# Kernel optimization log

Hardware: AMD Instinct MI355X
Metric: run time of the kernel (lower is better)

The kernel has to match this reference:

```python
import jax, jax.numpy as jnp
import numpy as np
from jax import lax

K = 16        # patch_size / kernel_size
S = 16        # stride
EMB = 768     # embed_dim
CIN = 3


def setup_inputs() -> dict:
    key = jax.random.key(0)
    k1, k2, k3, k4, k5 = jax.random.split(key, 5)
    B, H, W = 64, 384, 384
    pixel_values = jax.random.normal(k1, (B, CIN, H, W), jnp.float32)
    # offset conv: Conv2d(3, 2*K*K, kernel=K, stride=K); small init so offsets stay moderate
    offset_w = jax.random.normal(k2, (2 * K * K, CIN, K, K), jnp.float32) * 0.01
    offset_b = jax.random.normal(k3, (2 * K * K,), jnp.float32) * 0.01
    # deformable projection: DeformConv2d(3, 768, kernel=K, stride=K)
    proj_w = jax.random.normal(k4, (EMB, CIN, K, K), jnp.float32) * 0.02
    proj_b = jax.random.normal(k5, (EMB,), jnp.float32) * 0.02
    return {"pixel_values": pixel_values, "offset_w": offset_w, "offset_b": offset_b,
            "proj_w": proj_w, "proj_b": proj_b}


def _bilinear_gather(img, py, px):
    """img: [B,C,H,W]; py,px: [B,K,K,HO,WO] float sample coords.
    Returns [B,C,K,K,HO,WO] with zero padding outside the image (torchvision semantics)."""
    B, C, H, W = img.shape
    shp = py.shape
    y0 = jnp.floor(py); x0 = jnp.floor(px)
    wy1 = py - y0; wy0 = 1.0 - wy1
    wx1 = px - x0; wx0 = 1.0 - wx1
    imgf = img.reshape(B, C, H * W)

    def corner(yy, xx, w):
        valid = (yy >= 0) & (yy < H) & (xx >= 0) & (xx < W)
        yi = jnp.clip(yy, 0, H - 1).astype(jnp.int32)
        xi = jnp.clip(xx, 0, W - 1).astype(jnp.int32)
        idx = (yi * W + xi).reshape(B, -1)                       # [B, N]
        v = jnp.take_along_axis(imgf, idx[:, None, :], axis=2)   # [B, C, N]
        return v * (jnp.where(valid, w, 0.0)).reshape(B, 1, -1)

    val = (corner(y0, x0, wy0 * wx0) + corner(y0, x0 + 1, wy0 * wx1)
           + corner(y0 + 1, x0, wy1 * wx0) + corner(y0 + 1, x0 + 1, wy1 * wx1))
    return val.reshape((B, C) + shp[1:])


def reference(pixel_values, offset_w, offset_b, proj_w, proj_b):
    B, C, H, W = pixel_values.shape
    HO, WO = H // S, W // S
    # offset conv (dense, stride=patch, VALID padding)
    offset = lax.conv_general_dilated(pixel_values, offset_w, (S, S), 'VALID',
                                      dimension_numbers=('NCHW', 'OIHW', 'NCHW'))
    offset = offset + offset_b[None, :, None, None]              # [B, 2*K*K, HO, WO]
    off = offset.reshape(B, K * K, 2, HO, WO)
    dy = off[:, :, 0].reshape(B, K, K, HO, WO)
    dx = off[:, :, 1].reshape(B, K, K, HO, WO)
    # base sampling grid: p = (ho*S + i + dy, wo*S + j + dx)
    base_y = (jnp.arange(HO, dtype=jnp.float32) * S)[None, None, None, :, None] \
             + jnp.arange(K, dtype=jnp.float32)[None, :, None, None, None]
    base_x = (jnp.arange(WO, dtype=jnp.float32) * S)[None, None, None, None, :] \
             + jnp.arange(K, dtype=jnp.float32)[None, None, :, None, None]
    py = base_y + dy
    px = base_x + dx
    sampled = _bilinear_gather(pixel_values, py, px)             # [B, C, K, K, HO, WO]
    out = jnp.einsum('bcijhw,ocij->bohw', sampled, proj_w) + proj_b[None, :, None, None]
    # flatten(2).transpose(1,2) -> [B, HO*WO, EMB]
    return out.reshape(B, EMB, HO * WO).transpose(0, 2, 1)
```

## Files before the change

### kernel.cpp

```cpp
#include <hip/hip_runtime.h>
#include <stdint.h>

typedef __bf16 bf16x8 __attribute__((ext_vector_type(8)));
typedef float  f32x4  __attribute__((ext_vector_type(4)));

#define HH 384
#define WW 384
#define NPIX (HH*WW)
#define NC 3
#define NPATCH 576
#define EMB 768
#define PLEN 768
#define KSTEPS 24
#define NLOC (64*576)
#define W1_UNITS (32*KSTEPS*64)
#define W2_UNITS (48*KSTEPS*64)
#define W2_OFF   (W1_UNITS*8)
#define AP_OFF   ((W1_UNITS+W2_UNITS)*8)
#define SA_OFF   (AP_OFF + NLOC*PLEN)
#define P0_WBLKS ((W1_UNITS+W2_UNITS)/256)
#define P0_BANDS (64*24)

__device__ __forceinline__ uint16_t f2bf(float f) {
    uint32_t u = __builtin_bit_cast(uint32_t, f);
    u += 0x7FFFu + ((u >> 16) & 1u);
    return (uint16_t)(u >> 16);
}
__device__ __forceinline__ uint32_t pk2(float a, float b) {
    return (uint32_t)f2bf(a) | ((uint32_t)f2bf(b) << 16);
}
__device__ __forceinline__ float bf2f(uint16_t u) {
    return __builtin_bit_cast(float, (uint32_t)u << 16);
}

__global__ __launch_bounds__(256)
void p0_prepass(const float* __restrict__ offw, const float* __restrict__ projw,
                const float* __restrict__ pix, uint16_t* __restrict__ wz) {
    __shared__ uint16_t L[3 * 16 * 384];
    int b = blockIdx.x;
    if (b < P0_WBLKS) {
        int u = b * 256 + threadIdx.x;
        const float* src;
        int uu;
        if (u < W1_UNITS) { src = offw; uu = u; }
        else              { src = projw; uu = u - W1_UNITS; }
        int lane = uu & 63;
        int t    = uu >> 6;
        int ks   = t % KSTEPS;
        int nt   = t / KSTEPS;
        int n    = nt * 16 + (lane & 15);
        int k0   = ks * 32 + (lane >> 4) * 8;
        const float4* s4 = (const float4*)(src + (size_t)n * PLEN + k0);
        float4 v0 = s4[0], v1 = s4[1];
        uint4 w;
        w.x = pk2(v0.x, v0.y); w.y = pk2(v0.z, v0.w);
        w.z = pk2(v1.x, v1.y); w.w = pk2(v1.z, v1.w);
        *(uint4*)(wz + (size_t)u * 8) = w;
        return;
    }
    int band = b - P0_WBLKS;
    int img  = band / 24;
    int yb   = band - img * 24;
    const float* src = pix + (size_t)img * NC * NPIX + (size_t)yb * 16 * WW;
    #pragma unroll
    for (int i = 0; i < 18; ++i) {
        int u = threadIdx.x + i * 256;
        int c = u / 1536;
        int r = u - c * 1536;
        float4 v = *(const float4*)(src + (size_t)c * NPIX + (size_t)r * 4);
        uint2 o;
        o.x = pk2(v.x, v.y);
        o.y = pk2(v.z, v.w);
        *(uint2*)&L[c * 6144 + r * 4] = o;
    }
    __syncthreads();
    uint16_t* ap = wz + AP_OFF + (size_t)(img * NPATCH + yb * 24) * PLEN;
    #pragma unroll
    for (int i = 0; i < 9; ++i) {
        int u  = threadIdx.x + i * 256;
        int p  = u / 96;
        int k8 = (u - p * 96) * 8;
        int c  = k8 >> 8;
        int ii = (k8 >> 4) & 15;
        int j  = k8 & 15;
        uint4 d = *(const uint4*)&L[(c * 16 + ii) * 384 + p * 16 + j];
        *(uint4*)(ap + (size_t)p * PLEN + k8) = d;
    }
}

__global__ __launch_bounds__(256, 3)
void k1_offgemm(const uint16_t* __restrict__ wz, const float* __restrict__ offb,
                uint16_t* __restrict__ sa) {
    __shared__ __align__(16) uint16_t Asb[2][128][64];
    const int tid = threadIdx.x, wv = tid >> 6, lane = tid & 63;
    const int lr = lane & 15, lg = lane >> 4;
    const int wm = wv >> 1, wn = wv & 1;
    int bid = (int)blockIdx.x;
    const int fin   = (bid & 7) * 144 + (bid >> 3);
    const int mtile = fin >> 2;
    const int nc    = fin & 3;
    const int loc0  = mtile * 128;
    const int n0    = nc * 128;
    const uint16_t* __restrict__ Ap = wz + AP_OFF;

    const uint16_t* gs[4];
    #pragma unroll
    for (int l = 0; l < 4; ++l) {
        int u = l * 256 + tid;
        int row = u >> 3, ch = u & 7;
        gs[l] = Ap + (size_t)(loc0 + row) * PLEN + (ch ^ (row & 7)) * 8;
    }
    auto stage = [&](int t, int buf) {
        #pragma unroll
        for (int l = 0; l < 4; ++l)
            __builtin_amdgcn_global_load_lds(
                (const uint32_t*)(gs[l] + t * 64),
                (uint32_t*)((uint16_t*)&Asb[buf][0][0] + (size_t)(l * 256 + wv * 64) * 8),
                16, 0, 0);
    };
    auto ldb = [&](int nt, int ks) -> bf16x8 {
        int ntg = nc * 8 + wn * 4 + nt;
        return *(const bf16x8*)(wz + ((size_t)((ntg * KSTEPS + ks) * 64 + lane)) * 8);
    };

    f32x4 acc[4][4];
    #pragma unroll
    for (int nt = 0; nt < 4; ++nt) {
        float bz = offb[n0 + wn * 64 + nt * 16 + lr];
        f32x4 z = {bz, bz, bz, bz};
        #pragma unroll
        for (int mi = 0; mi < 4; ++mi) acc[mi][nt] = z;
    }

    bf16x8 ba[4], bb[4];
    stage(0, 0);
    #pragma unroll
    for (int nt = 0; nt < 4; ++nt) ba[nt] = ldb(nt, 0);
    __syncthreads();

    #pragma unroll 1
    for (int t = 0; t < 12; ++t) {
        const int cur = t & 1;
        if (t < 11) stage(t + 1, cur ^ 1);
        {
            #pragma unroll
            for (int nt = 0; nt < 4; ++nt) bb[nt] = ldb(nt, 2 * t + 1);
            const int u0 = (lg ^ (lr & 7)) * 8;
            bf16x8 a0 = *(const bf16x8*)&Asb[cur][wm * 64 +  0 + lr][u0];
            bf16x8 a1 = *(const bf16x8*)&Asb[cur][wm * 64 + 16 + lr][u0];
            bf16x8 a2 = *(const bf16x8*)&Asb[cur][wm * 64 + 32 + lr][u0];
            bf16x8 a3 = *(const bf16x8*)&Asb[cur][wm * 64 + 48 + lr][u0];
            #pragma unroll
            for (int nt = 0; nt < 4; ++nt) {
                acc[0][nt] = __builtin_amdgcn_mfma_f32_16x16x32_bf16(a0, ba[nt], acc[0][nt], 0, 0, 0);
                acc[1][nt] = __builtin_amdgcn_mfma_f32_16x16x32_bf16(a1, ba[nt], acc[1][nt], 0, 0, 0);
                acc[2][nt] = __builtin_amdgcn_mfma_f32_16x16x32_bf16(a2, ba[nt], acc[2][nt], 0, 0, 0);
                acc[3][nt] = __builtin_amdgcn_mfma_f32_16x16x32_bf16(a3, ba[nt], acc[3][nt], 0, 0, 0);
            }
        }
        {
            if (t < 11) {
                #pragma unroll
                for (int nt = 0; nt < 4; ++nt) ba[nt] = ldb(nt, 2 * t + 2);
            }
            const int u1 = ((4 + lg) ^ (lr & 7)) * 8;
            bf16x8 a0 = *(const bf16x8*)&Asb[cur][wm * 64 +  0 + lr][u1];
            bf16x8 a1 = *(const bf16x8*)&Asb[cur][wm * 64 + 16 + lr][u1];
            bf16x8 a2 = *(const bf16x8*)&Asb[cur][wm * 64 + 32 + lr][u1];
            bf16x8 a3 = *(const bf16x8*)&Asb[cur][wm * 64 + 48 + lr][u1];
            #pragma unroll
            for (int nt = 0; nt < 4; ++nt) {
                acc[0][nt] = __builtin_amdgcn_mfma_f32_16x16x32_bf16(a0, bb[nt], acc[0][nt], 0, 0, 0);
                acc[1][nt] = __builtin_amdgcn_mfma_f32_16x16x32_bf16(a1, bb[nt], acc[1][nt], 0, 0, 0);
                acc[2][nt] = __builtin_amdgcn_mfma_f32_16x16x32_bf16(a2, bb[nt], acc[2][nt], 0, 0, 0);
                acc[3][nt] = __builtin_amdgcn_mfma_f32_16x16x32_bf16(a3, bb[nt], acc[3][nt], 0, 0, 0);
            }
        }
        __syncthreads();
    }

    #pragma unroll
    for (int nt = 0; nt < 4; ++nt)
      #pragma unroll
      for (int mi = 0; mi < 4; ++mi)
        #pragma unroll
        for (int r = 0; r < 4; ++r) {
            float v  = acc[mi][nt][r];
            float pv = __shfl_xor(v, 1);
            if ((lane & 1) == 0) {
                int row = loc0 + wm * 64 + mi * 16 + lg * 4 + r;
                int q   = (n0 >> 1) + wn * 32 + nt * 8 + (lr >> 1);
                ((uint32_t*)(sa + (size_t)row * PLEN))[q] = pk2(v, pv);
            }
        }
}

__global__ __launch_bounds__(512)
void k2_gather(const uint16_t* __restrict__ wz, uint16_t* __restrict__ sa) {
    const int tid  = threadIdx.x;
    const int wv   = tid >> 6;
    const int lane = tid & 63;
    int bid = (int)blockIdx.x;
    const int tile = (bid & 7) * 144 + (bid >> 3);
    const int loc0 = tile * 32;
    const int bimg = loc0 / NPATCH;
    const int p0   = loc0 - bimg * NPATCH;
    const uint16_t* __restrict__ apim = wz + AP_OFF + (size_t)bimg * NPATCH * PLEN;

    #pragma unroll
    for (int li = 0; li < 4; ++li) {
        const int L   = wv * 4 + li;
        const int p   = p0 + L;
        const int ho  = p / 24;
        const int wo  = p - ho * 24;
        const int by  = ho * 16;
        const int bx  = wo * 16;
        uint16_t* row = sa + (size_t)(loc0 + L) * PLEN;
        const uint32_t* rowu = (const uint32_t*)row;
        uint32_t od0 = rowu[       lane];
        uint32_t od1 = rowu[ 64 +  lane];
        uint32_t od2 = rowu[128 +  lane];
        uint32_t od3 = rowu[192 +  lane];
        asm volatile("s_waitcnt vmcnt(0)" ::: "memory");
        #pragma unroll
        for (int s4 = 0; s4 < 4; ++s4) {
            const int q  = s4 * 64 + lane;
            const int qi = q >> 4;
            const int qj = q & 15;
            uint32_t od = (s4 == 0) ? od0 : (s4 == 1) ? od1 : (s4 == 2) ? od2 : od3;
            float dy = bf2f((uint16_t)od);
            float dx = bf2f((uint16_t)(od >> 16));
            float py = (float)(by + qi) + dy;
            float px = (float)(bx + qj) + dx;
            float y0f = floorf(py), x0f = floorf(px);
            float wy1 = py - y0f, wy0 = 1.f - wy1;
            float wx1 = px - x0f, wx0 = 1.f - wx1;
            int y0 = (int)y0f, x0 = (int)x0f;
            float s0 = 0.f, s1 = 0.f, s2 = 0.f;
            #pragma unroll
            for (int cy = 0; cy < 2; ++cy) {
                int yy = y0 + cy;
                if ((unsigned)yy < (unsigned)HH) {
                    float wy = cy ? wy1 : wy0;
                    #pragma unroll
                    for (int cx = 0; cx < 2; ++cx) {
                        int xx = x0 + cx;
                        if ((unsigned)xx < (unsigned)WW) {
                            float w = wy * (cx ? wx1 : wx0);
                            int pp = (yy >> 4) * 24 + (xx >> 4);
                            const uint16_t* cp = apim + (size_t)pp * PLEN
                                               + (((yy & 15) << 4) | (xx & 15));
                            s0 += w * bf2f(cp[0]);
                            s1 += w * bf2f(cp[256]);
                            s2 += w * bf2f(cp[512]);
                        }
                    }
                }
            }
            row[      q] = f2bf(s0);
            row[256 + q] = f2bf(s1);
            row[512 + q] = f2bf(s2);
        }
    }
}

__global__ __launch_bounds__(256, 3)
void k3_proj(const uint16_t* __restrict__ wz, const float* __restrict__ projb,
             float* __restrict__ out) {
    __shared__ __align__(16) uint16_t Asb[2][128][64];
    const int tid = threadIdx.x, wv = tid >> 6, lane = tid & 63;
    const int lr = lane & 15, lg = lane >> 4;
    const int wm = wv >> 1, wn = wv & 1;
    int bid = (int)blockIdx.x;
    const int fin   = (bid & 7) * 216 + (bid >> 3);
    const int mtile = fin / 6;
    const int ncol  = fin - mtile * 6;
    const int loc0  = mtile * 128;
    const int n0    = ncol * 128;
    const uint16_t* __restrict__ sa = wz + SA_OFF;

    const uint16_t* gs[4];
    #pragma unroll
    for (int l = 0; l < 4; ++l) {
        int u = l * 256 + tid;
        int row = u >> 3, ch = u & 7;
        gs[l] = sa + (size_t)(loc0 + row) * PLEN + (ch ^ (row & 7)) * 8;
    }
    auto stage = [&](int t, int buf) {
        #pragma unroll
        for (int l = 0; l < 4; ++l)
            __builtin_amdgcn_global_load_lds(
                (const uint32_t*)(gs[l] + t * 64),
                (uint32_t*)((uint16_t*)&Asb[buf][0][0] + (size_t)(l * 256 + wv * 64) * 8),
                16, 0, 0);
    };
    auto ldb = [&](int nt, int ks) -> bf16x8 {
        int ntg = ncol * 8 + wn * 4 + nt;
        return *(const bf16x8*)(wz + W2_OFF + ((size_t)((ntg * KSTEPS + ks) * 64 + lane)) * 8);
    };

    f32x4 acc[4][4];
    #pragma unroll
    for (int nt = 0; nt < 4; ++nt) {
        float bz = projb[n0 + wn * 64 + nt * 16 + lr];
        f32x4 z = {bz, bz, bz, bz};
        #pragma unroll
        for (int mi = 0; mi < 4; ++mi) acc[mi][nt] = z;
    }

    bf16x8 ba[4], bb[4];
    stage(0, 0);
    #pragma unroll
    for (int nt = 0; nt < 4; ++nt) ba[nt] = ldb(nt, 0);
    __syncthreads();

    #pragma unroll 1
    for (int t = 0; t < 12; ++t) {
        const int cur = t & 1;
        if (t < 11) stage(t + 1, cur ^ 1);
        {
            #pragma unroll
            for (int nt = 0; nt < 4; ++nt) bb[nt] = ldb(nt, 2 * t + 1);
            const int u0 = (lg ^ (lr & 7)) * 8;
            bf16x8 a0 = *(const bf16x8*)&Asb[cur][wm * 64 +  0 + lr][u0];
            bf16x8 a1 = *(const bf16x8*)&Asb[cur][wm * 64 + 16 + lr][u0];
            bf16x8 a2 = *(const bf16x8*)&Asb[cur][wm * 64 + 32 + lr][u0];
            bf16x8 a3 = *(const bf16x8*)&Asb[cur][wm * 64 + 48 + lr][u0];
            #pragma unroll
            for (int nt = 0; nt < 4; ++nt) {
                acc[0][nt] = __builtin_amdgcn_mfma_f32_16x16x32_bf16(a0, ba[nt], acc[0][nt], 0, 0, 0);
                acc[1][nt] = __builtin_amdgcn_mfma_f32_16x16x32_bf16(a1, ba[nt], acc[1][nt], 0, 0, 0);
                acc[2][nt] = __builtin_amdgcn_mfma_f32_16x16x32_bf16(a2, ba[nt], acc[2][nt], 0, 0, 0);
                acc[3][nt] = __builtin_amdgcn_mfma_f32_16x16x32_bf16(a3, ba[nt], acc[3][nt], 0, 0, 0);
            }
        }
        {
            if (t < 11) {
                #pragma unroll
                for (int nt = 0; nt < 4; ++nt) ba[nt] = ldb(nt, 2 * t + 2);
            }
            const int u1 = ((4 + lg) ^ (lr & 7)) * 8;
            bf16x8 a0 = *(const bf16x8*)&Asb[cur][wm * 64 +  0 + lr][u1];
            bf16x8 a1 = *(const bf16x8*)&Asb[cur][wm * 64 + 16 + lr][u1];
            bf16x8 a2 = *(const bf16x8*)&Asb[cur][wm * 64 + 32 + lr][u1];
            bf16x8 a3 = *(const bf16x8*)&Asb[cur][wm * 64 + 48 + lr][u1];
            #pragma unroll
            for (int nt = 0; nt < 4; ++nt) {
                acc[0][nt] = __builtin_amdgcn_mfma_f32_16x16x32_bf16(a0, bb[nt], acc[0][nt], 0, 0, 0);
                acc[1][nt] = __builtin_amdgcn_mfma_f32_16x16x32_bf16(a1, bb[nt], acc[1][nt], 0, 0, 0);
                acc[2][nt] = __builtin_amdgcn_mfma_f32_16x16x32_bf16(a2, bb[nt], acc[2][nt], 0, 0, 0);
                acc[3][nt] = __builtin_amdgcn_mfma_f32_16x16x32_bf16(a3, bb[nt], acc[3][nt], 0, 0, 0);
            }
        }
        __syncthreads();
    }

    #pragma unroll
    for (int mi = 0; mi < 4; ++mi)
      #pragma unroll
      for (int r = 0; r < 4; ++r) {
        int rowg = loc0 + wm * 64 + mi * 16 + lg * 4 + r;
        float* op = out + (size_t)rowg * EMB + n0 + wn * 64;
        #pragma unroll
        for (int nt = 0; nt < 4; ++nt)
            op[nt * 16 + lr] = acc[mi][nt][r];
      }
}

__global__ __launch_bounds__(256)
void fallback_kernel(const float* __restrict__ pix, const float* __restrict__ offw,
                     const float* __restrict__ offb, const float* __restrict__ projw,
                     const float* __restrict__ projb, float* __restrict__ out) {
    __shared__ float buf[8][PLEN];
    const int tid = threadIdx.x;
    const int loc0 = blockIdx.x * 8;
    #pragma unroll
    for (int r = 0; r < 6; ++r) {
        int item = tid + r * 256;
        int l = item / 192, k = (item - l * 192) * 4;
        int c = k >> 8, i = (k >> 4) & 15, j = k & 15;
        int flat = loc0 + l, b = flat / NPATCH, p = flat - b * NPATCH;
        int ho = p / 24, wo = p - ho * 24;
        *(float4*)(&buf[l][k]) = *(const float4*)(pix +
            (((size_t)b * NC + c) * HH + (size_t)ho * 16 + i) * WW + wo * 16 + j);
    }
    __syncthreads();
    float dy[8], dx[8];
    {
        float a0[8], a1[8];
        float b0 = offb[2 * tid], b1 = offb[2 * tid + 1];
        #pragma unroll
        for (int l = 0; l < 8; ++l) { a0[l] = b0; a1[l] = b1; }
        const float4* w0 = (const float4*)(offw + (size_t)(2 * tid) * PLEN);
        const float4* w1 = w0 + PLEN / 4;
        for (int k4 = 0; k4 < PLEN / 4; ++k4) {
            float4 wa = w0[k4], wb = w1[k4];
            #pragma unroll
            for (int l = 0; l < 8; ++l) {
                float4 pv = *(const float4*)(&buf[l][k4 * 4]);
                a0[l] += wa.x*pv.x + wa.y*pv.y + wa.z*pv.z + wa.w*pv.w;
                a1[l] += wb.x*pv.x + wb.y*pv.y + wb.z*pv.z + wb.w*pv.w;
            }
        }
        #pragma unroll
        for (int l = 0; l < 8; ++l) { dy[l] = a0[l]; dx[l] = a1[l]; }
    }
    __syncthreads();
    {
        const int i = tid >> 4, j = tid & 15;
        #pragma unroll
        for (int l = 0; l < 8; ++l) {
            int flat = loc0 + l, b = flat / NPATCH, p = flat - b * NPATCH;
            int ho = p / 24, wo = p - ho * 24;
            float py = (float)(ho * 16 + i) + dy[l];
            float px = (float)(wo * 16 + j) + dx[l];
            float y0 = floorf(py), x0 = floorf(px);
            float wy1 = py - y0, wy0 = 1.f - wy1, wx1 = px - x0, wx0 = 1.f - wx1;
            const float* pb = pix + (size_t)b * NC * NPIX;
            float s0 = 0, s1 = 0, s2 = 0;
            #pragma unroll
            for (int cy = 0; cy < 2; ++cy)
              #pragma unroll
              for (int cx = 0; cx < 2; ++cx) {
                int yy = (int)y0 + cy, xx = (int)x0 + cx;
                float w = (cy ? wy1 : wy0) * (cx ? wx1 : wx0);
                if ((unsigned)yy < (unsigned)HH && (unsigned)xx < (unsigned)WW) {
                    int idx = yy * WW + xx;
                    s0 += w * pb[idx]; s1 += w * pb[NPIX + idx]; s2 += w * pb[2*NPIX + idx];
                }
              }
            buf[l][tid] = s0; buf[l][256 + tid] = s1; buf[l][512 + tid] = s2;
        }
    }
    __syncthreads();
    {
        float aA[8], aB[8], aC[8];
        float bA = projb[tid], bB = projb[tid + 256], bC = projb[tid + 512];
        #pragma unroll
        for (int l = 0; l < 8; ++l) { aA[l] = bA; aB[l] = bB; aC[l] = bC; }
        const float4* wA = (const float4*)(projw + (size_t)tid * PLEN);
        const float4* wB = (const float4*)(projw + (size_t)(tid + 256) * PLEN);
        const float4* wC = (const float4*)(projw + (size_t)(tid + 512) * PLEN);
        for (int k4 = 0; k4 < PLEN / 4; ++k4) {
            float4 a = wA[k4], bq = wB[k4], cq = wC[k4];
            #pragma unroll
            for (int l = 0; l < 8; ++l) {
                float4 pv = *(const float4*)(&buf[l][k4 * 4]);
                aA[l] += a.x*pv.x + a.y*pv.y + a.z*pv.z + a.w*pv.w;
                aB[l] += bq.x*pv.x + bq.y*pv.y + bq.z*pv.z + bq.w*pv.w;
                aC[l] += cq.x*pv.x + cq.y*pv.y + cq.z*pv.z + cq.w*pv.w;
            }
        }
        #pragma unroll
        for (int l = 0; l < 8; ++l) {
            float* op = out + (size_t)(loc0 + l) * EMB;
            op[tid] = aA[l]; op[tid + 256] = aB[l]; op[tid + 512] = aC[l];
        }
    }
}

extern "C" void kernel_launch(void* const* d_in, const int* in_sizes, int n_in,
                              void* d_out, int out_size, void* d_ws, size_t ws_size,
                              hipStream_t stream) {
    const float* pix   = (const float*)d_in[0];
    const float* offw  = (const float*)d_in[1];
    const float* offb  = (const float*)d_in[2];
    const float* projw = (const float*)d_in[3];
    const float* projb = (const float*)d_in[4];
    float* out = (float*)d_out;
    uint16_t* wz = (uint16_t*)d_ws;

    const size_t ws_needed = ((size_t)SA_OFF + (size_t)NLOC * PLEN) * 2;

    if (ws_size >= ws_needed) {
        uint16_t* sa = wz + SA_OFF;
        p0_prepass<<<P0_WBLKS + P0_BANDS, 256, 0, stream>>>(offw, projw, pix, wz);
        k1_offgemm<<<1152, 256, 0, stream>>>(wz, offb, sa);
        k2_gather<<<1152, 512, 0, stream>>>(wz, sa);
        k3_proj<<<1728, 256, 0, stream>>>(wz, projb, out);
    } else {
        fallback_kernel<<<NLOC / 8, 256, 0, stream>>>(pix, offw, offb, projw, projb, out);
    }
}
```

Baseline: 205.2 us.

## Interleave channels in patch layout so bilinear gather loads all three in two words

Changes the K dimension ordering of the patch matrix and offset weights from channel-major (c*256+q) to channel-interleaved (q*3+c), applied consistently in the prepass for both the offset weights and the pixel patches. The bilinear sampler can then fetch all three channels of a corner with two adjacent 32-bit loads instead of three loads spaced 512 bytes apart. In exchange the prepass does scalar strided LDS reads and scalar global loads for the offset weights rather than vector loads, and the sampler adds shift and select logic for odd alignment.

```diff
diff --git a/kernel.cpp b/kernel.cpp
--- a/kernel.cpp
+++ b/kernel.cpp
@@ -40,22 +40,41 @@
     int b = blockIdx.x;
     if (b < P0_WBLKS) {
         int u = b * 256 + threadIdx.x;
-        const float* src;
-        int uu;
-        if (u < W1_UNITS) { src = offw; uu = u; }
-        else              { src = projw; uu = u - W1_UNITS; }
-        int lane = uu & 63;
-        int t    = uu >> 6;
-        int ks   = t % KSTEPS;
-        int nt   = t / KSTEPS;
-        int n    = nt * 16 + (lane & 15);
-        int k0   = ks * 32 + (lane >> 4) * 8;
-        const float4* s4 = (const float4*)(src + (size_t)n * PLEN + k0);
-        float4 v0 = s4[0], v1 = s4[1];
-        uint4 w;
-        w.x = pk2(v0.x, v0.y); w.y = pk2(v0.z, v0.w);
-        w.z = pk2(v1.x, v1.y); w.w = pk2(v1.z, v1.w);
-        *(uint4*)(wz + (size_t)u * 8) = w;
+        int lane = u & 63;
+        if (u < W1_UNITS) {
+            int t  = u >> 6;
+            int ks = t % KSTEPS;
+            int nt = t / KSTEPS;
+            int n  = nt * 16 + (lane & 15);
+            int k0 = ks * 32 + (lane >> 4) * 8;
+            const float* src = offw + (size_t)n * PLEN;
+            uint16_t tmp[8];
+            #pragma unroll
+            for (int e = 0; e < 8; ++e) {
+                int k = k0 + e;
+                int q = k / 3, c = k - q * 3;
+                tmp[e] = f2bf(src[c * 256 + q]);
+            }
+            uint4 w;
+            w.x = tmp[0] | ((uint32_t)tmp[1] << 16);
+            w.y = tmp[2] | ((uint32_t)tmp[3] << 16);
+            w.z = tmp[4] | ((uint32_t)tmp[5] << 16);
+            w.w = tmp[6] | ((uint32_t)tmp[7] << 16);
+            *(uint4*)(wz + (size_t)u * 8) = w;
+        } else {
+            int uu = u - W1_UNITS;
+            int t2 = uu >> 6;
+            int ks = t2 % KSTEPS;
+            int nt = t2 / KSTEPS;
+            int n  = nt * 16 + (lane & 15);
+            int k0 = ks * 32 + (lane >> 4) * 8;
+            const float4* s4 = (const float4*)(projw + (size_t)n * PLEN + k0);
+            float4 v0 = s4[0], v1 = s4[1];
+            uint4 w;
+            w.x = pk2(v0.x, v0.y); w.y = pk2(v0.z, v0.w);
+            w.z = pk2(v1.x, v1.y); w.w = pk2(v1.z, v1.w);
+            *(uint4*)(wz + (size_t)u * 8) = w;
+        }
         return;
     }
     int band = b - P0_WBLKS;
@@ -80,10 +99,19 @@
         int u  = threadIdx.x + i * 256;
         int p  = u / 96;
         int k8 = (u - p * 96) * 8;
-        int c  = k8 >> 8;
-        int ii = (k8 >> 4) & 15;
-        int j  = k8 & 15;
-        uint4 d = *(const uint4*)&L[(c * 16 + ii) * 384 + p * 16 + j];
+        uint16_t tmp[8];
+        #pragma unroll
+        for (int e = 0; e < 8; ++e) {
+            int k = k8 + e;
+            int q = k / 3, c = k - q * 3;
+            int ii = q >> 4, j = q & 15;
+            tmp[e] = L[(c * 16 + ii) * 384 + p * 16 + j];
+        }
+        uint4 d;
+        d.x = tmp[0] | ((uint32_t)tmp[1] << 16);
+        d.y = tmp[2] | ((uint32_t)tmp[3] << 16);
+        d.z = tmp[4] | ((uint32_t)tmp[5] << 16);
+        d.w = tmp[6] | ((uint32_t)tmp[7] << 16);
         *(uint4*)(ap + (size_t)p * PLEN + k8) = d;
     }
 }
@@ -247,12 +275,17 @@
                         int xx = x0 + cx;
                         if ((unsigned)xx < (unsigned)WW) {
                             float w = wy * (cx ? wx1 : wx0);
-                            int pp = (yy >> 4) * 24 + (xx >> 4);
-                            const uint16_t* cp = apim + (size_t)pp * PLEN
-                                               + (((yy & 15) << 4) | (xx & 15));
-                            s0 += w * bf2f(cp[0]);
-                            s1 += w * bf2f(cp[256]);
-                            s2 += w * bf2f(cp[512]);
+                            int pp   = (yy >> 4) * 24 + (xx >> 4);
+                            int elem = ((((yy & 15) << 4) | (xx & 15))) * 3;
+                            const uint32_t* rp = (const uint32_t*)(apim + (size_t)pp * PLEN);
+                            uint32_t lo32 = rp[elem >> 1];
+                            uint32_t hi32 = rp[(elem >> 1) + 1];
+                            bool odd = (elem & 1);
+                            uint32_t pair01 = odd ? ((lo32 >> 16) | (hi32 << 16)) : lo32;
+                            uint32_t c2b    = odd ? (hi32 & 0xFFFF0000u) : (hi32 << 16);
+                            s0 += w * __builtin_bit_cast(float, pair01 << 16);
+                            s1 += w * __builtin_bit_cast(float, pair01 & 0xFFFF0000u);
+                            s2 += w * __builtin_bit_cast(float, c2b);
                         }
                     }
                 }
```

Measured after the change: 194.5 us. -5.2%, faster.
